# Optimization experiments

Measured on AMD Instinct MI355X. Metric: run time of the kernel, lower is better.

Reference implementation:

```python
import jax, jax.numpy as jnp
import numpy as np

N_NODES = 50000
N_EDGES = 800000
IN_FEAT = 128
HID = 64
HEADS = 4
OUT = 40
NEG_SLOPE = 0.2


def _p(key, shape, scale=0.05):
    return jax.random.normal(key, shape, dtype=jnp.float32) * scale


def setup_inputs() -> dict:
    key = jax.random.key(0)
    ks = jax.random.split(key, 20)
    HW = HID * HEADS  # 256
    inp = {
        "x": jax.random.normal(ks[0], (N_NODES, IN_FEAT), dtype=jnp.float32),
        "edge_index": jax.random.randint(ks[1], (2, N_EDGES), 0, N_NODES, dtype=jnp.int64),
        # GATConv 1: in=128 -> heads=4, C=64
        "W1": _p(ks[2], (IN_FEAT, HW)), "as1": _p(ks[3], (HEADS, HID)), "ad1": _p(ks[4], (HEADS, HID)), "b1": jnp.zeros((HW,), jnp.float32),
        # GATConv 2: in=256
        "W2": _p(ks[5], (HW, HW)), "as2": _p(ks[6], (HEADS, HID)), "ad2": _p(ks[7], (HEADS, HID)), "b2": jnp.zeros((HW,), jnp.float32),
        # GATConv 3: in=256
        "W3": _p(ks[8], (HW, HW)), "as3": _p(ks[9], (HEADS, HID)), "ad3": _p(ks[10], (HEADS, HID)), "b3": jnp.zeros((HW,), jnp.float32),
        # MLP head: Linear(256,256) + Linear(256,40)
        "Wm1": _p(ks[11], (HW, HW)), "bm1": jnp.zeros((HW,), jnp.float32),
        "Wm2": _p(ks[12], (HW, OUT)), "bm2": jnp.zeros((OUT,), jnp.float32),
    }
    return inp


def gat_conv(x, src, dst, W, a_src, a_dst, bias, num_nodes):
    """PyG GATConv: concat=True, add_self_loops=True, leaky_relu(0.2)."""
    H, C = a_src.shape
    h = (x @ W).reshape(num_nodes, H, C)            # [N,H,C]
    # per-node attention logits (computed once, gathered per edge)
    src_logit = jnp.einsum('nhc,hc->nh', h, a_src)  # [N,H]
    dst_logit = jnp.einsum('nhc,hc->nh', h, a_dst)  # [N,H]
    # add self loops
    loop = jnp.arange(num_nodes, dtype=src.dtype)
    s = jnp.concatenate([src, loop])
    d = jnp.concatenate([dst, loop])
    alpha = jax.nn.leaky_relu(src_logit[s] + dst_logit[d], NEG_SLOPE)  # [E,H]
    # segment softmax over incoming edges of each destination node
    amax = jax.ops.segment_max(alpha, d, num_segments=num_nodes)
    e = jnp.exp(alpha - amax[d])
    denom = jax.ops.segment_sum(e, d, num_segments=num_nodes)
    coef = e / denom[d]                              # [E,H]
    msg = h[s] * coef[:, :, None]                    # [E,H,C] gather+weight
    out = jax.ops.segment_sum(msg, d, num_segments=num_nodes)  # [N,H,C]
    return out.reshape(num_nodes, H * C) + bias


def reference(x, edge_index, W1, as1, ad1, b1, W2, as2, ad2, b2, W3, as3, ad3, b3, Wm1, bm1, Wm2, bm2):
    src, dst = edge_index[0], edge_index[1]
    n = x.shape[0]
    h = jax.nn.relu(gat_conv(x, src, dst, W1, as1, ad1, b1, n))
    h = jax.nn.relu(gat_conv(h, src, dst, W2, as2, ad2, b2, n))
    h = jax.nn.relu(gat_conv(h, src, dst, W3, as3, ad3, b3, n))
    h = jax.nn.relu(h @ Wm1 + bm1)
    return h @ Wm2 + bm2
```

## Files before the change

kernel.cpp:

```cpp
#include <hip/hip_runtime.h>


constexpr int NN = 50000;
constexpr int NE = 800000;
constexpr int NN_PAD = 50176;
constexpr int CAP = 48;

typedef _Float16 f16x8 __attribute__((ext_vector_type(8)));
typedef _Float16 f16x4 __attribute__((ext_vector_type(4)));
typedef float    f32x4 __attribute__((ext_vector_type(4)));

__device__ __forceinline__ void cp16(void* lds, const void* g)
{
    __builtin_amdgcn_global_load_lds(
        (const __attribute__((address_space(1))) uint32_t*)g,
        (__attribute__((address_space(3))) uint32_t*)lds, 16, 0, 0);
}

constexpr int CVT_BLKS = 944;
__global__ __launch_bounds__(256)
void prep_kernel(const float* __restrict__ W1, const float* __restrict__ W2,
                 const float* __restrict__ W3, const float* __restrict__ Wm1,
                 const float* __restrict__ Wm2,
                 _Float16* B1h, _Float16* B1l, _Float16* B2h, _Float16* B2l,
                 _Float16* B3h, _Float16* B3l, _Float16* Bmh, _Float16* Bml,
                 _Float16* Whh, _Float16* Whl,
                 const int* __restrict__ src, const int* __restrict__ dst,
                 int* __restrict__ cursor, int* __restrict__ bucket)
{
    if (blockIdx.x >= CVT_BLKS) {
        int e = ((int)blockIdx.x - CVT_BLKS) * 256 + (int)threadIdx.x;
        if (e >= NE) return;
        int d = dst[e];
        int pos = atomicAdd(&cursor[d], 1);
        if (pos < CAP) bucket[d * CAP + pos] = src[e];
        return;
    }
    int idx = blockIdx.x * 256 + (int)threadIdx.x;
    const float* W; _Float16 *H, *Lo; int K, local;
    if (idx < 32768)       { W = W1;  H = B1h; Lo = B1l; K = 128; local = idx; }
    else if (idx < 98304)  { W = W2;  H = B2h; Lo = B2l; K = 256; local = idx - 32768; }
    else if (idx < 163840) { W = W3;  H = B3h; Lo = B3l; K = 256; local = idx - 98304; }
    else if (idx < 229376) { W = Wm1; H = Bmh; Lo = Bml; K = 256; local = idx - 163840; }
    else if (idx < 241664) {
        int l = idx - 229376; int n = l >> 8, k = l & 255;
        float v = (n < 40) ? Wm2[k * 40 + n] : 0.f;
        _Float16 h = (_Float16)v;
        Whh[l] = h; Whl[l] = (_Float16)(v - (float)h);
        return;
    } else return;
    int k = local >> 8, n = local & 255;
    float v = W[local];
    _Float16 h = (_Float16)v;
    H[n * K + k] = h;
    Lo[n * K + k] = (_Float16)(v - (float)h);
}

template<bool FUSE, bool PRESPLIT, bool EMIT_SPLIT>
__global__ __launch_bounds__(512, 4)
void gemm_mfma(const float* __restrict__ A,
               const _Float16* Ah, const _Float16* Al,
               const _Float16* __restrict__ Bhi, const _Float16* __restrict__ Blo,
               const float* __restrict__ bias,
               _Float16* __restrict__ h16, _Float16* __restrict__ h16lo,
               _Float16* Oh, _Float16* Ol,
               const float* __restrict__ a_src, const float* __restrict__ a_dst,
               float* __restrict__ sl, float* __restrict__ dl,
               int M, int K)
{
    __shared__ __align__(16) _Float16 sAhi[2][128][32], sAlo[2][128][32];
    __shared__ __align__(16) _Float16 sBhi[256][32], sBlo[256][32];

    const int tid  = (int)threadIdx.x;
    const int wave = tid >> 6;
    const int mw   = wave >> 2;
    const int nw   = wave & 3;
    const int lane = tid & 63;
    const int l15  = lane & 15;
    const int quad = lane >> 4;
    const int swz  = (l15 >> 1) & 3;
    const int bm   = blockIdx.x * 128;

    f32x4 acc[4][4];
    #pragma unroll
    for (int i = 0; i < 4; ++i)
        #pragma unroll
        for (int j = 0; j < 4; ++j)
            acc[i][j] = (f32x4){0.f, 0.f, 0.f, 0.f};

    auto stageA_dma = [&](int b, int k0) {
        int rowA = wave * 16 + (lane >> 2);
        int c = (lane & 3) ^ ((rowA >> 1) & 3);
        cp16(&sAhi[b][wave * 16][0], Ah + (size_t)(bm + rowA) * K + k0 + c * 8);
        cp16(&sAlo[b][wave * 16][0], Al + (size_t)(bm + rowA) * K + k0 + c * 8);
    };
    auto stageB = [&](int k0) {
        int pos = lane & 3;
        #pragma unroll
        for (int j = 0; j < 2; ++j) {
            int rowB = wave * 32 + j * 16 + (lane >> 2);
            int c = pos ^ ((rowB >> 1) & 3);
            cp16(&sBhi[wave * 32 + j * 16][0], Bhi + (size_t)rowB * K + k0 + c * 8);
            cp16(&sBlo[wave * 32 + j * 16][0], Blo + (size_t)rowB * K + k0 + c * 8);
        }
    };
    const int ar = tid >> 2, ac = tid & 3;
    auto writeA_cvt = [&](int b, float4 v0, float4 v1) {
        float fv[8] = {v0.x, v0.y, v0.z, v0.w, v1.x, v1.y, v1.z, v1.w};
        f16x8 h8, l8;
        #pragma unroll
        for (int u = 0; u < 8; ++u) {
            _Float16 hh = (_Float16)fv[u];
            h8[u] = hh; l8[u] = (_Float16)(fv[u] - (float)hh);
        }
        int slot = (ac ^ ((ar >> 1) & 3)) * 8;
        *(f16x8*)&sAhi[b][ar][slot] = h8;
        *(f16x8*)&sAlo[b][ar][slot] = l8;
    };
    auto loadA32 = [&](int k0, float4& v0, float4& v1) {
        int grow = bm + ar;
        v0 = make_float4(0.f, 0.f, 0.f, 0.f); v1 = v0;
        if (grow < M) {
            v0 = *(const float4*)(A + (size_t)grow * K + k0 + ac * 8);
            v1 = *(const float4*)(A + (size_t)grow * K + k0 + ac * 8 + 4);
        }
    };

    if (PRESPLIT) {
        stageA_dma(0, 0);
    } else {
        float4 v0, v1;
        loadA32(0, v0, v1);
        writeA_cvt(0, v0, v1);
    }
    stageB(0);
    __syncthreads();

    const int NT = K >> 5;
    for (int t = 0; t < NT; ++t) {
        const int cb = t & 1, nb = cb ^ 1;
        const bool pf = (t + 1 < NT);
        const int kn = (t + 1) << 5;

        float4 pv0, pv1;
        if (pf) {
            if (PRESPLIT) stageA_dma(nb, kn);
            else          loadA32(kn, pv0, pv1);
        }

        f16x8 bh[4], bl[4];
        #pragma unroll
        for (int nt = 0; nt < 4; ++nt) {
            int n = nw * 64 + nt * 16 + l15;
            bh[nt] = *(const f16x8*)&sBhi[n][(quad ^ swz) * 8];
            bl[nt] = *(const f16x8*)&sBlo[n][(quad ^ swz) * 8];
        }
        #pragma unroll
        for (int mt = 0; mt < 4; ++mt) {
            int m = mw * 64 + mt * 16 + l15;
            f16x8 ah = *(const f16x8*)&sAhi[cb][m][(quad ^ swz) * 8];
            f16x8 al = *(const f16x8*)&sAlo[cb][m][(quad ^ swz) * 8];
            #pragma unroll
            for (int nt = 0; nt < 4; ++nt) {
                acc[mt][nt] = __builtin_amdgcn_mfma_f32_16x16x32_f16(ah, bh[nt], acc[mt][nt], 0, 0, 0);
                acc[mt][nt] = __builtin_amdgcn_mfma_f32_16x16x32_f16(al, bh[nt], acc[mt][nt], 0, 0, 0);
                acc[mt][nt] = __builtin_amdgcn_mfma_f32_16x16x32_f16(ah, bl[nt], acc[mt][nt], 0, 0, 0);
            }
        }

        if (pf && !PRESPLIT) writeA_cvt(nb, pv0, pv1);

        if (pf) {
            __syncthreads();
            stageB(kn);
            __syncthreads();
        }
    }

    float aS[4], aD[4];
    if (FUSE) {
        #pragma unroll
        for (int nt = 0; nt < 4; ++nt) {
            aS[nt] = a_src[nw * 64 + nt * 16 + l15];
            aD[nt] = a_dst[nw * 64 + nt * 16 + l15];
        }
    }

    #pragma unroll
    for (int mt = 0; mt < 4; ++mt) {
        #pragma unroll
        for (int r = 0; r < 4; ++r) {
            int row = bm + mw * 64 + mt * 16 + quad * 4 + r;
            bool ok = (row < M);
            if (ok) {
                #pragma unroll
                for (int nt = 0; nt < 4; ++nt) {
                    int col = nw * 64 + nt * 16 + l15;
                    float c = acc[mt][nt][r];
                    if (EMIT_SPLIT) {
                        float v = fmaxf(c + bias[col], 0.f);
                        _Float16 hh = (_Float16)v;
                        Oh[(size_t)row * 256 + col] = hh;
                        Ol[(size_t)row * 256 + col] = (_Float16)(v - (float)hh);
                    } else {
                        _Float16 hh = (_Float16)c;
                        h16[(size_t)row * 256 + col] = hh;
                        h16lo[(size_t)row * 256 + col] = (_Float16)(c - (float)hh);
                    }
                }
            }
            if (FUSE) {
                float vs = 0.f, vd = 0.f;
                #pragma unroll
                for (int nt = 0; nt < 4; ++nt) {
                    float c = acc[mt][nt][r];
                    vs = fmaf(c, aS[nt], vs);
                    vd = fmaf(c, aD[nt], vd);
                }
                #pragma unroll
                for (int off = 8; off >= 1; off >>= 1) {
                    vs += __shfl_xor(vs, off, 64);
                    vd += __shfl_xor(vd, off, 64);
                }
                if (l15 == 0 && ok) {
                    sl[row * 4 + nw] = vs;
                    dl[row * 4 + nw] = vd;
                }
            }
        }
    }
}

__global__ __launch_bounds__(256)
void gemm_head(const _Float16* __restrict__ Ah, const _Float16* __restrict__ Al,
               const _Float16* __restrict__ Bh, const _Float16* __restrict__ Bl,
               const float* __restrict__ bias, float* __restrict__ out, int M)
{
    __shared__ _Float16 sAhi[256][40], sAlo[256][40];
    __shared__ _Float16 sBhi[48][40],  sBlo[48][40];

    const int tid  = (int)threadIdx.x;
    const int wave = tid >> 6;
    const int lane = tid & 63;
    const int l15  = lane & 15;
    const int quad = lane >> 4;
    const int bm   = blockIdx.x * 256;

    f32x4 acc[4][3];
    #pragma unroll
    for (int i = 0; i < 4; ++i)
        #pragma unroll
        for (int j = 0; j < 3; ++j)
            acc[i][j] = (f32x4){0.f, 0.f, 0.f, 0.f};

    for (int k0 = 0; k0 < 256; k0 += 32) {
        #pragma unroll
        for (int i = 0; i < 4; ++i) {
            int idx = tid + i * 256;
            int row = idx >> 2, kq = (idx & 3) * 8;
            int grow = bm + row;
            uint4 vh = {0,0,0,0}, vl = {0,0,0,0};
            if (grow < M) {
                vh = *(const uint4*)(Ah + (size_t)grow * 256 + k0 + kq);
                vl = *(const uint4*)(Al + (size_t)grow * 256 + k0 + kq);
            }
            *(uint4*)&sAhi[row][kq] = vh;
            *(uint4*)&sAlo[row][kq] = vl;
        }
        if (tid < 192) {
            int n = tid >> 2, kq = (tid & 3) * 8;
            *(uint4*)&sBhi[n][kq] = *(const uint4*)(Bh + (size_t)n * 256 + k0 + kq);
            *(uint4*)&sBlo[n][kq] = *(const uint4*)(Bl + (size_t)n * 256 + k0 + kq);
        }
        __syncthreads();

        f16x8 bh[3], bl[3];
        #pragma unroll
        for (int nt = 0; nt < 3; ++nt) {
            int n = nt * 16 + l15;
            bh[nt] = *(const f16x8*)&sBhi[n][quad * 8];
            bl[nt] = *(const f16x8*)&sBlo[n][quad * 8];
        }
        #pragma unroll
        for (int mt = 0; mt < 4; ++mt) {
            int m = wave * 64 + mt * 16 + l15;
            f16x8 ah = *(const f16x8*)&sAhi[m][quad * 8];
            f16x8 al = *(const f16x8*)&sAlo[m][quad * 8];
            #pragma unroll
            for (int nt = 0; nt < 3; ++nt) {
                acc[mt][nt] = __builtin_amdgcn_mfma_f32_16x16x32_f16(ah, bh[nt], acc[mt][nt], 0, 0, 0);
                acc[mt][nt] = __builtin_amdgcn_mfma_f32_16x16x32_f16(al, bh[nt], acc[mt][nt], 0, 0, 0);
                acc[mt][nt] = __builtin_amdgcn_mfma_f32_16x16x32_f16(ah, bl[nt], acc[mt][nt], 0, 0, 0);
            }
        }
        __syncthreads();
    }

    #pragma unroll
    for (int mt = 0; mt < 4; ++mt) {
        #pragma unroll
        for (int r = 0; r < 4; ++r) {
            int row = bm + wave * 64 + mt * 16 + quad * 4 + r;
            if (row >= M) continue;
            #pragma unroll
            for (int nt = 0; nt < 3; ++nt) {
                int col = nt * 16 + l15;
                if (col < 40)
                    out[(size_t)row * 40 + col] = acc[mt][nt][r] + bias[col];
            }
        }
    }
}

__device__ __forceinline__ float leaky02(float a) {
    return (a >= 0.f) ? a : 0.2f * a;
}

__global__ __launch_bounds__(256)
void gat_aggregate(const int* __restrict__ cursor, const int* __restrict__ bucket,
                   const float* __restrict__ sl, const float* __restrict__ dl,
                   const _Float16* __restrict__ h16, const _Float16* __restrict__ h16lo,
                   const float* __restrict__ bias,
                   _Float16* __restrict__ Ph, _Float16* __restrict__ Pl)
{
    __shared__ __align__(16) float sE[4][CAP][4];
    __shared__ __align__(16) int   sIdx[4][CAP];

    const int wv = (int)threadIdx.x >> 6;
    const int n = blockIdx.x * 4 + wv;
    if (n >= NN) return;
    const int lane = (int)threadIdx.x & 63;
    const int head = lane >> 4;
    const int cnt = min(cursor[n], CAP);

    if (lane < cnt) {
        int s = bucket[(size_t)n * CAP + lane];
        sIdx[wv][lane] = s;
        float4 s4 = *(const float4*)(sl + s * 4);
        float4 d4 = *(const float4*)(dl + n * 4);
        float4 e4;
        e4.x = __expf(leaky02(s4.x + d4.x));
        e4.y = __expf(leaky02(s4.y + d4.y));
        e4.z = __expf(leaky02(s4.z + d4.z));
        e4.w = __expf(leaky02(s4.w + d4.w));
        *(float4*)&sE[wv][lane][0] = e4;
    }

    const float dlh = dl[n * 4 + head];
    float exs = __expf(leaky02(sl[n * 4 + head] + dlh));
    f16x4 shi = *(const f16x4*)(h16   + (size_t)n * 256 + lane * 4);
    f16x4 slo = *(const f16x4*)(h16lo + (size_t)n * 256 + lane * 4);
    float4 a0; float d0 = exs;
    a0.x = exs * ((float)shi[0] + (float)slo[0]);
    a0.y = exs * ((float)shi[1] + (float)slo[1]);
    a0.z = exs * ((float)shi[2] + (float)slo[2]);
    a0.w = exs * ((float)shi[3] + (float)slo[3]);
    float4 a1 = {0,0,0,0}, a2 = {0,0,0,0}, a3 = {0,0,0,0};
    float d1 = 0.f, d2 = 0.f, d3 = 0.f;

    const int vo = lane * 4;
    int i = 0;
    for (; i + 3 < cnt; i += 4) {
        int s0 = __builtin_amdgcn_readfirstlane(sIdx[wv][i]);
        int s1 = __builtin_amdgcn_readfirstlane(sIdx[wv][i + 1]);
        int s2 = __builtin_amdgcn_readfirstlane(sIdx[wv][i + 2]);
        int s3 = __builtin_amdgcn_readfirstlane(sIdx[wv][i + 3]);
        float e0 = sE[wv][i][head];
        float e1 = sE[wv][i + 1][head];
        float e2 = sE[wv][i + 2][head];
        float e3 = sE[wv][i + 3][head];
        f16x4 h0 = *(const f16x4*)(h16 + ((size_t)(uint32_t)s0 << 8) + vo);
        f16x4 h1 = *(const f16x4*)(h16 + ((size_t)(uint32_t)s1 << 8) + vo);
        f16x4 h2 = *(const f16x4*)(h16 + ((size_t)(uint32_t)s2 << 8) + vo);
        f16x4 h3 = *(const f16x4*)(h16 + ((size_t)(uint32_t)s3 << 8) + vo);
        a0.x = fmaf(e0, (float)h0[0], a0.x); a0.y = fmaf(e0, (float)h0[1], a0.y);
        a0.z = fmaf(e0, (float)h0[2], a0.z); a0.w = fmaf(e0, (float)h0[3], a0.w);
        d0 += e0;
        a1.x = fmaf(e1, (float)h1[0], a1.x); a1.y = fmaf(e1, (float)h1[1], a1.y);
        a1.z = fmaf(e1, (float)h1[2], a1.z); a1.w = fmaf(e1, (float)h1[3], a1.w);
        d1 += e1;
        a2.x = fmaf(e2, (float)h2[0], a2.x); a2.y = fmaf(e2, (float)h2[1], a2.y);
        a2.z = fmaf(e2, (float)h2[2], a2.z); a2.w = fmaf(e2, (float)h2[3], a2.w);
        d2 += e2;
        a3.x = fmaf(e3, (float)h3[0], a3.x); a3.y = fmaf(e3, (float)h3[1], a3.y);
        a3.z = fmaf(e3, (float)h3[2], a3.z); a3.w = fmaf(e3, (float)h3[3], a3.w);
        d3 += e3;
    }
    for (; i < cnt; ++i) {
        int s0 = __builtin_amdgcn_readfirstlane(sIdx[wv][i]);
        float e0 = sE[wv][i][head];
        f16x4 h0 = *(const f16x4*)(h16 + ((size_t)(uint32_t)s0 << 8) + vo);
        a0.x = fmaf(e0, (float)h0[0], a0.x); a0.y = fmaf(e0, (float)h0[1], a0.y);
        a0.z = fmaf(e0, (float)h0[2], a0.z); a0.w = fmaf(e0, (float)h0[3], a0.w);
        d0 += e0;
    }
    float4 acc;
    acc.x = (a0.x + a1.x) + (a2.x + a3.x);
    acc.y = (a0.y + a1.y) + (a2.y + a3.y);
    acc.z = (a0.z + a1.z) + (a2.z + a3.z);
    acc.w = (a0.w + a1.w) + (a2.w + a3.w);
    float denom = (d0 + d1) + (d2 + d3);

    float inv = 1.f / denom;
    float4 bv = *(const float4*)(bias + lane * 4);
    float rv[4];
    rv[0] = fmaxf(bv.x + acc.x * inv, 0.f);
    rv[1] = fmaxf(bv.y + acc.y * inv, 0.f);
    rv[2] = fmaxf(bv.z + acc.z * inv, 0.f);
    rv[3] = fmaxf(bv.w + acc.w * inv, 0.f);
    f16x4 h, l;
    #pragma unroll
    for (int u = 0; u < 4; ++u) {
        _Float16 hh = (_Float16)rv[u];
        h[u] = hh; l[u] = (_Float16)(rv[u] - (float)hh);
    }
    *(f16x4*)(Ph + (size_t)n * 256 + vo) = h;
    *(f16x4*)(Pl + (size_t)n * 256 + vo) = l;
}

extern "C" void kernel_launch(void* const* d_in, const int* in_sizes, int n_in,
                              void* d_out, int out_size, void* d_ws, size_t ws_size,
                              hipStream_t stream)
{
    const float* x   = (const float*)d_in[0];
    const int*   ei  = (const int*)d_in[1];
    const int* src = ei;
    const int* dst = ei + NE;
    const float* W1  = (const float*)d_in[2];
    const float* as1 = (const float*)d_in[3];
    const float* ad1 = (const float*)d_in[4];
    const float* b1  = (const float*)d_in[5];
    const float* W2  = (const float*)d_in[6];
    const float* as2 = (const float*)d_in[7];
    const float* ad2 = (const float*)d_in[8];
    const float* b2  = (const float*)d_in[9];
    const float* W3  = (const float*)d_in[10];
    const float* as3 = (const float*)d_in[11];
    const float* ad3 = (const float*)d_in[12];
    const float* b3  = (const float*)d_in[13];
    const float* Wm1 = (const float*)d_in[14];
    const float* bm1 = (const float*)d_in[15];
    const float* Wm2 = (const float*)d_in[16];
    const float* bm2 = (const float*)d_in[17];
    float* out = (float*)d_out;

    float* ws  = (float*)d_ws;
    float* sl  = ws;
    float* dl  = sl + NN * 4;
    int* cursor = (int*)(dl + NN * 4);
    int* bucket = cursor + NN;
    uintptr_t fb = (uintptr_t)(bucket + (size_t)NN * CAP);
    fb = (fb + 15) & ~(uintptr_t)15;
    _Float16* wb = (_Float16*)fb;
    _Float16* B1h = wb;                 _Float16* B1l = B1h + 256 * 128;
    _Float16* B2h = B1l + 256 * 128;    _Float16* B2l = B2h + 256 * 256;
    _Float16* B3h = B2l + 256 * 256;    _Float16* B3l = B3h + 256 * 256;
    _Float16* Bmh = B3l + 256 * 256;    _Float16* Bml = Bmh + 256 * 256;
    _Float16* Whh = Bml + 256 * 256;    _Float16* Whl = Whh + 48 * 256;
    _Float16* H16  = Whl + 48 * 256;
    _Float16* H16l = H16 + (size_t)NN * 256;
    _Float16* Ph  = H16l + (size_t)NN * 256;
    _Float16* Pl  = Ph   + (size_t)NN_PAD * 256;

    const dim3 block(256);
    const dim3 block512(512);
    const dim3 mfmaGrid((NN + 127) / 128);
    const dim3 headGrid((NN + 255) / 256);
    const int prepBlocks = CVT_BLKS + (NE + 255) / 256;
    const int aggBlocks = (NN + 3) / 4;

    (void)hipMemsetAsync(cursor, 0, (size_t)NN * sizeof(int), stream);
    prep_kernel<<<prepBlocks, block, 0, stream>>>(
        W1, W2, W3, Wm1, Wm2, B1h, B1l, B2h, B2l, B3h, B3l, Bmh, Bml, Whh, Whl,
        src, dst, cursor, bucket);

    gemm_mfma<true, false, false><<<mfmaGrid, block512, 0, stream>>>(
        x, nullptr, nullptr, B1h, B1l, nullptr, H16, H16l, nullptr, nullptr,
        as1, ad1, sl, dl, NN, 128);
    gat_aggregate<<<aggBlocks, block, 0, stream>>>(cursor, bucket, sl, dl, H16, H16l, b1, Ph, Pl);

    gemm_mfma<true, true, false><<<mfmaGrid, block512, 0, stream>>>(
        nullptr, Ph, Pl, B2h, B2l, nullptr, H16, H16l, nullptr, nullptr,
        as2, ad2, sl, dl, NN, 256);
    gat_aggregate<<<aggBlocks, block, 0, stream>>>(cursor, bucket, sl, dl, H16, H16l, b2, Ph, Pl);

    gemm_mfma<true, true, false><<<mfmaGrid, block512, 0, stream>>>(
        nullptr, Ph, Pl, B3h, B3l, nullptr, H16, H16l, nullptr, nullptr,
        as3, ad3, sl, dl, NN, 256);
    gat_aggregate<<<aggBlocks, block, 0, stream>>>(cursor, bucket, sl, dl, H16, H16l, b3, Ph, Pl);

    gemm_mfma<false, true, true><<<mfmaGrid, block512, 0, stream>>>(
        nullptr, Ph, Pl, Bmh, Bml, bm1, nullptr, nullptr, Ph, Pl,
        nullptr, nullptr, nullptr, nullptr, NN, 256);
    gemm_head<<<headGrid, block, 0, stream>>>(Ph, Pl, Whh, Whl, bm2, out, NN);
}
```

Baseline: 568.3 us.

## Fuse MLP head into last GEMM and move edge scatter into first GEMM launch

The output head Linear(256,40) is computed inside the Wm1 GEMM epilogue. The ReLU'd tile is staged in shared memory and reduced across waves with LDS atomics, so the Ph/Pl round trip and the separate gemm_head launch go away. The edge bucketing scatter moves from prep_kernel into extra blocks of the first GEMM launch, so it can overlap with GEMM work. In exchange the epilogue adds extra syncs and shared-memory atomics per m-tile, and the scatter now depends on the first GEMM grid.

```diff
diff --git a/kernel.cpp b/kernel.cpp
--- a/kernel.cpp
+++ b/kernel.cpp
@@ -5,6 +5,8 @@
 constexpr int NE = 800000;
 constexpr int NN_PAD = 50176;
 constexpr int CAP = 48;
+constexpr int GEMM_BLKS = (NN + 127) / 128;
+constexpr int SCAT_BLKS = (NE + 511) / 512;
 
 typedef _Float16 f16x8 __attribute__((ext_vector_type(8)));
 typedef _Float16 f16x4 __attribute__((ext_vector_type(4)));
@@ -24,18 +26,8 @@
                  const float* __restrict__ Wm2,
                  _Float16* B1h, _Float16* B1l, _Float16* B2h, _Float16* B2l,
                  _Float16* B3h, _Float16* B3l, _Float16* Bmh, _Float16* Bml,
-                 _Float16* Whh, _Float16* Whl,
-                 const int* __restrict__ src, const int* __restrict__ dst,
-                 int* __restrict__ cursor, int* __restrict__ bucket)
+                 _Float16* Whh, _Float16* Whl)
 {
-    if (blockIdx.x >= CVT_BLKS) {
-        int e = ((int)blockIdx.x - CVT_BLKS) * 256 + (int)threadIdx.x;
-        if (e >= NE) return;
-        int d = dst[e];
-        int pos = atomicAdd(&cursor[d], 1);
-        if (pos < CAP) bucket[d * CAP + pos] = src[e];
-        return;
-    }
     int idx = blockIdx.x * 256 + (int)threadIdx.x;
     const float* W; _Float16 *H, *Lo; int K, local;
     if (idx < 32768)       { W = W1;  H = B1h; Lo = B1l; K = 128; local = idx; }
@@ -56,22 +48,36 @@
     Lo[n * K + k] = (_Float16)(v - (float)h);
 }
 
-template<bool FUSE, bool PRESPLIT, bool EMIT_SPLIT>
+template<bool FUSE, bool PRESPLIT, bool HEADF, bool SCATTER>
 __global__ __launch_bounds__(512, 4)
 void gemm_mfma(const float* __restrict__ A,
                const _Float16* Ah, const _Float16* Al,
                const _Float16* __restrict__ Bhi, const _Float16* __restrict__ Blo,
                const float* __restrict__ bias,
                _Float16* __restrict__ h16, _Float16* __restrict__ h16lo,
-               _Float16* Oh, _Float16* Ol,
+               const _Float16* __restrict__ Wh_hi, const _Float16* __restrict__ Wh_lo,
+               const float* __restrict__ bias2, float* __restrict__ out,
                const float* __restrict__ a_src, const float* __restrict__ a_dst,
                float* __restrict__ sl, float* __restrict__ dl,
+               const int* __restrict__ e_src, const int* __restrict__ e_dst,
+               int* __restrict__ cursor, int* __restrict__ bucket,
                int M, int K)
 {
     __shared__ __align__(16) _Float16 sAhi[2][128][32], sAlo[2][128][32];
     __shared__ __align__(16) _Float16 sBhi[256][32], sBlo[256][32];
 
     const int tid  = (int)threadIdx.x;
+
+    if (SCATTER && (int)blockIdx.x >= GEMM_BLKS) {
+        int e = ((int)blockIdx.x - GEMM_BLKS) * 512 + tid;
+        if (e < NE) {
+            int d = e_dst[e];
+            int pos = atomicAdd(&cursor[d], 1);
+            if (pos < CAP) bucket[d * CAP + pos] = e_src[e];
+        }
+        return;
+    }
+
     const int wave = tid >> 6;
     const int mw   = wave >> 2;
     const int nw   = wave & 3;
@@ -177,6 +183,73 @@
         }
     }
 
+    if (HEADF) {
+        _Float16* hH = (_Float16*)&sAhi[0][0][0];
+        _Float16* hL = (_Float16*)&sAlo[0][0][0];
+        float* redf  = (float*)&sBhi[0][0];
+        const int mh = wave & 1, kq = wave >> 1;
+        __syncthreads();
+        for (int mt = 0; mt < 4; ++mt) {
+            #pragma unroll
+            for (int r = 0; r < 4; ++r) {
+                int lrow = mw * 16 + quad * 4 + r;
+                #pragma unroll
+                for (int nt = 0; nt < 4; ++nt) {
+                    int col = nw * 64 + nt * 16 + l15;
+                    float v = fmaxf(acc[mt][nt][r] + bias[col], 0.f);
+                    _Float16 hh = (_Float16)v;
+                    hH[lrow * 256 + col] = hh;
+                    hL[lrow * 256 + col] = (_Float16)(v - (float)hh);
+                }
+            }
+            for (int z = tid; z < 2 * 3 * 16 * 17; z += 512) redf[z] = 0.f;
+            __syncthreads();
+            f32x4 a3[3];
+            #pragma unroll
+            for (int nt = 0; nt < 3; ++nt) a3[nt] = (f32x4){0.f, 0.f, 0.f, 0.f};
+            #pragma unroll
+            for (int kc = 0; kc < 2; ++kc) {
+                int k0 = kq * 64 + kc * 32;
+                f16x8 ah = *(const f16x8*)&hH[(mh * 16 + l15) * 256 + k0 + quad * 8];
+                f16x8 al = *(const f16x8*)&hL[(mh * 16 + l15) * 256 + k0 + quad * 8];
+                #pragma unroll
+                for (int nt = 0; nt < 3; ++nt) {
+                    int n = nt * 16 + l15;
+                    f16x8 bh = *(const f16x8*)(Wh_hi + n * 256 + k0 + quad * 8);
+                    f16x8 bl = *(const f16x8*)(Wh_lo + n * 256 + k0 + quad * 8);
+                    a3[nt] = __builtin_amdgcn_mfma_f32_16x16x32_f16(ah, bh, a3[nt], 0, 0, 0);
+                    a3[nt] = __builtin_amdgcn_mfma_f32_16x16x32_f16(al, bh, a3[nt], 0, 0, 0);
+                    a3[nt] = __builtin_amdgcn_mfma_f32_16x16x32_f16(ah, bl, a3[nt], 0, 0, 0);
+                }
+            }
+            #pragma unroll
+            for (int nt = 0; nt < 3; ++nt)
+                #pragma unroll
+                for (int rg = 0; rg < 4; ++rg)
+                    atomicAdd(&redf[((mh * 3 + nt) * 16 + l15) * 17 + quad * 4 + rg],
+                              a3[nt][rg]);
+            __syncthreads();
+            if (kq == 0) {
+                #pragma unroll
+                for (int rg = 0; rg < 4; ++rg) {
+                    int grow = bm + mh * 64 + mt * 16 + quad * 4 + rg;
+                    if (grow < M) {
+                        #pragma unroll
+                        for (int nt = 0; nt < 3; ++nt) {
+                            int col = nt * 16 + l15;
+                            if (col < 40)
+                                out[(size_t)grow * 40 + col] =
+                                    redf[((mh * 3 + nt) * 16 + l15) * 17 + quad * 4 + rg]
+                                    + bias2[col];
+                        }
+                    }
+                }
+            }
+            __syncthreads();
+        }
+        return;
+    }
+
     float aS[4], aD[4];
     if (FUSE) {
         #pragma unroll
@@ -197,16 +270,9 @@
                 for (int nt = 0; nt < 4; ++nt) {
                     int col = nw * 64 + nt * 16 + l15;
                     float c = acc[mt][nt][r];
-                    if (EMIT_SPLIT) {
-                        float v = fmaxf(c + bias[col], 0.f);
-                        _Float16 hh = (_Float16)v;
-                        Oh[(size_t)row * 256 + col] = hh;
-                        Ol[(size_t)row * 256 + col] = (_Float16)(v - (float)hh);
-                    } else {
-                        _Float16 hh = (_Float16)c;
-                        h16[(size_t)row * 256 + col] = hh;
-                        h16lo[(size_t)row * 256 + col] = (_Float16)(c - (float)hh);
-                    }
+                    _Float16 hh = (_Float16)c;
+                    h16[(size_t)row * 256 + col] = hh;
+                    h16lo[(size_t)row * 256 + col] = (_Float16)(c - (float)hh);
                 }
             }
             if (FUSE) {
@@ -226,87 +292,6 @@
                     sl[row * 4 + nw] = vs;
                     dl[row * 4 + nw] = vd;
                 }
-            }
-        }
-    }
-}
-
-__global__ __launch_bounds__(256)
-void gemm_head(const _Float16* __restrict__ Ah, const _Float16* __restrict__ Al,
-               const _Float16* __restrict__ Bh, const _Float16* __restrict__ Bl,
-               const float* __restrict__ bias, float* __restrict__ out, int M)
-{
-    __shared__ _Float16 sAhi[256][40], sAlo[256][40];
-    __shared__ _Float16 sBhi[48][40],  sBlo[48][40];
-
-    const int tid  = (int)threadIdx.x;
-    const int wave = tid >> 6;
-    const int lane = tid & 63;
-    const int l15  = lane & 15;
-    const int quad = lane >> 4;
-    const int bm   = blockIdx.x * 256;
-
-    f32x4 acc[4][3];
-    #pragma unroll
-    for (int i = 0; i < 4; ++i)
-        #pragma unroll
-        for (int j = 0; j < 3; ++j)
-            acc[i][j] = (f32x4){0.f, 0.f, 0.f, 0.f};
-
-    for (int k0 = 0; k0 < 256; k0 += 32) {
-        #pragma unroll
-        for (int i = 0; i < 4; ++i) {
-            int idx = tid + i * 256;
-            int row = idx >> 2, kq = (idx & 3) * 8;
-            int grow = bm + row;
-            uint4 vh = {0,0,0,0}, vl = {0,0,0,0};
-            if (grow < M) {
-                vh = *(const uint4*)(Ah + (size_t)grow * 256 + k0 + kq);
-                vl = *(const uint4*)(Al + (size_t)grow * 256 + k0 + kq);
-            }
-            *(uint4*)&sAhi[row][kq] = vh;
-            *(uint4*)&sAlo[row][kq] = vl;
-        }
-        if (tid < 192) {
-            int n = tid >> 2, kq = (tid & 3) * 8;
-            *(uint4*)&sBhi[n][kq] = *(const uint4*)(Bh + (size_t)n * 256 + k0 + kq);
-            *(uint4*)&sBlo[n][kq] = *(const uint4*)(Bl + (size_t)n * 256 + k0 + kq);
-        }
-        __syncthreads();
-
-        f16x8 bh[3], bl[3];
-        #pragma unroll
-        for (int nt = 0; nt < 3; ++nt) {
-            int n = nt * 16 + l15;
-            bh[nt] = *(const f16x8*)&sBhi[n][quad * 8];
-            bl[nt] = *(const f16x8*)&sBlo[n][quad * 8];
-        }
-        #pragma unroll
-        for (int mt = 0; mt < 4; ++mt) {
-            int m = wave * 64 + mt * 16 + l15;
-            f16x8 ah = *(const f16x8*)&sAhi[m][quad * 8];
-            f16x8 al = *(const f16x8*)&sAlo[m][quad * 8];
-            #pragma unroll
-            for (int nt = 0; nt < 3; ++nt) {
-                acc[mt][nt] = __builtin_amdgcn_mfma_f32_16x16x32_f16(ah, bh[nt], acc[mt][nt], 0, 0, 0);
-                acc[mt][nt] = __builtin_amdgcn_mfma_f32_16x16x32_f16(al, bh[nt], acc[mt][nt], 0, 0, 0);
-                acc[mt][nt] = __builtin_amdgcn_mfma_f32_16x16x32_f16(ah, bl[nt], acc[mt][nt], 0, 0, 0);
-            }
-        }
-        __syncthreads();
-    }
-
-    #pragma unroll
-    for (int mt = 0; mt < 4; ++mt) {
-        #pragma unroll
-        for (int r = 0; r < 4; ++r) {
-            int row = bm + wave * 64 + mt * 16 + quad * 4 + r;
-            if (row >= M) continue;
-            #pragma unroll
-            for (int nt = 0; nt < 3; ++nt) {
-                int col = nt * 16 + l15;
-                if (col < 40)
-                    out[(size_t)row * 40 + col] = acc[mt][nt][r] + bias[col];
             }
         }
     }
@@ -464,33 +449,35 @@
 
     const dim3 block(256);
     const dim3 block512(512);
-    const dim3 mfmaGrid((NN + 127) / 128);
-    const dim3 headGrid((NN + 255) / 256);
-    const int prepBlocks = CVT_BLKS + (NE + 255) / 256;
+    const dim3 g1Grid(GEMM_BLKS + SCAT_BLKS);
+    const dim3 mfmaGrid(GEMM_BLKS);
     const int aggBlocks = (NN + 3) / 4;
 
     (void)hipMemsetAsync(cursor, 0, (size_t)NN * sizeof(int), stream);
-    prep_kernel<<<prepBlocks, block, 0, stream>>>(
-        W1, W2, W3, Wm1, Wm2, B1h, B1l, B2h, B2l, B3h, B3l, Bmh, Bml, Whh, Whl,
-        src, dst, cursor, bucket);
-
-    gemm_mfma<true, false, false><<<mfmaGrid, block512, 0, stream>>>(
-        x, nullptr, nullptr, B1h, B1l, nullptr, H16, H16l, nullptr, nullptr,
-        as1, ad1, sl, dl, NN, 128);
+    prep_kernel<<<CVT_BLKS, block, 0, stream>>>(
+        W1, W2, W3, Wm1, Wm2, B1h, B1l, B2h, B2l, B3h, B3l, Bmh, Bml, Whh, Whl);
+
+    gemm_mfma<true, false, false, true><<<g1Grid, block512, 0, stream>>>(
+        x, nullptr, nullptr, B1h, B1l, nullptr, H16, H16l,
+        nullptr, nullptr, nullptr, nullptr,
+        as1, ad1, sl, dl, src, dst, cursor, bucket, NN, 128);
     gat_aggregate<<<aggBlocks, block, 0, stream>>>(cursor, bucket, sl, dl, H16, H16l, b1, Ph, Pl);
 
-    gemm_mfma<true, true, false><<<mfmaGrid, block512, 0, stream>>>(
-        nullptr, Ph, Pl, B2h, B2l, nullptr, H16, H16l, nullptr, nullptr,
-        as2, ad2, sl, dl, NN, 256);
+    gemm_mfma<true, true, false, false><<<mfmaGrid, block512, 0, stream>>>(
+        nullptr, Ph, Pl, B2h, B2l, nullptr, H16, H16l,
+        nullptr, nullptr, nullptr, nullptr,
+        as2, ad2, sl, dl, nullptr, nullptr, nullptr, nullptr, NN, 256);
     gat_aggregate<<<aggBlocks, block, 0, stream>>>(cursor, bucket, sl, dl, H16, H16l, b2, Ph, Pl);
 
-    gemm_mfma<true, true, false><<<mfmaGrid, block512, 0, stream>>>(
-        nullptr, Ph, Pl, B3h, B3l, nullptr, H16, H16l, nullptr, nullptr,
-        as3, ad3, sl, dl, NN, 256);
+    gemm_mfma<true, true, false, false><<<mfmaGrid, block512, 0, stream>>>(
+        nullptr, Ph, Pl, B3h, B3l, nullptr, H16, H16l,
+        nullptr, nullptr, nullptr, nullptr,
+        as3, ad3, sl, dl, nullptr, nullptr, nullptr, nullptr, NN, 256);
     gat_aggregate<<<aggBlocks, block, 0, stream>>>(cursor, bucket, sl, dl, H16, H16l, b3, Ph, Pl);
 
-    gemm_mfma<false, true, true><<<mfmaGrid, block512, 0, stream>>>(
-        nullptr, Ph, Pl, Bmh, Bml, bm1, nullptr, nullptr, Ph, Pl,
-        nullptr, nullptr, nullptr, nullptr, NN, 256);
-    gemm_head<<<headGrid, block, 0, stream>>>(Ph, Pl, Whh, Whl, bm2, out, NN);
-}
+    gemm_mfma<false, true, true, false><<<mfmaGrid, block512, 0, stream>>>(
+        nullptr, Ph, Pl, Bmh, Bml, bm1, nullptr, nullptr,
+        Whh, Whl, bm2, out,
+        nullptr, nullptr, nullptr, nullptr, nullptr, nullptr, nullptr, nullptr,
+        NN, 256);
+}
```

New measurement: 589.5 us. 3.7% more time.
